# Kernel optimization log

Measured on AMD Instinct MI355X. Metric: run time of the kernel, lower is better.

Reference implementation:

```python
import jax, jax.numpy as jnp
import numpy as np

EPSILON = 0.1
TAU = 1.0
NORM_EPS = 1e-12  # matches torch.nn.functional.normalize eps


def setup_inputs() -> dict:
    key = jax.random.key(0)
    k_ids, k_emb = jax.random.split(key)
    B, T, V, D = 2, 2048, 50257, 768
    input_ids = jax.random.randint(k_ids, (B, T), 0, V, dtype=jnp.int64)
    embedding_weight = jax.random.normal(k_emb, (V, D), dtype=jnp.float32)
    return {"input_ids": input_ids, "embedding_weight": embedding_weight}


def _l2_normalize(x):
    # F.normalize(p=2): x / max(||x||, eps)
    n = jnp.linalg.norm(x, axis=-1, keepdims=True)
    return x / jnp.maximum(n, NORM_EPS)


def reference(input_ids, embedding_weight):
    B, T = input_ids.shape
    V, D = embedding_weight.shape
    # embedding lookup -> (B*T, D)
    vecs = embedding_weight[input_ids].reshape(B * T, D)
    vectors_norm = _l2_normalize(vecs)
    embed_norm = _l2_normalize(embedding_weight)
    # (B*T, V) similarity, scaled by epsilon/2
    scaled_sim = (vectors_norm @ embed_norm.T) * (EPSILON / 2.0)
    # gumbel_softmax (soft, tau=1): softmax((logits + gumbel) / tau)
    gkey = jax.random.key(42)
    gumbel = jax.random.gumbel(gkey, scaled_sim.shape, dtype=scaled_sim.dtype)
    weights = jax.nn.softmax((scaled_sim + gumbel) / TAU, axis=1)
    # mix back through the (unnormalized) embedding table -> (B, T, D)
    selected = weights @ embedding_weight
    return selected.reshape(B, T, D)
```

## Files before the change

### kernel.cpp

```cpp
#include <hip/hip_runtime.h>
#include <stdint.h>

constexpr int VOC  = 50257;
constexpr int VPAD = 50304;
constexpr int DEMB = 768;
constexpr int NQ   = 4096;
constexpr float EPS_HALF = 0.05f;
constexpr float LOG2E = 1.4426950408889634f;
constexpr float C16   = -23.083120654223414f;

typedef __attribute__((ext_vector_type(4))) short    short4_t;
typedef __attribute__((ext_vector_type(8))) short    short8_t;
typedef __attribute__((ext_vector_type(4))) float    float4_t;
typedef __attribute__((ext_vector_type(4))) uint32_t uint4_t;

__device__ __forceinline__ short f2bf(float f) {
  uint32_t u = __float_as_uint(f);
  u += 0x7FFFu + ((u >> 16) & 1u);
  return (short)(u >> 16);
}

__device__ __forceinline__ void tf8(uint32_t e0, uint32_t out[8]) {
  const uint32_t K0 = 0u, K1 = 42u, K2 = 0x1BD11BDAu ^ 42u;
  uint32_t x0[8], x1[8];
#pragma unroll
  for (int r = 0; r < 8; ++r) { x0[r] = K0; x1[r] = e0 + (uint32_t)r + K1; }
#define R8(a) _Pragma("unroll") \
  for (int r = 0; r < 8; ++r) { x0[r] += x1[r]; x1[r] = __builtin_rotateleft32(x1[r], a) ^ x0[r]; }
#define INJ8(a, b, i) _Pragma("unroll") \
  for (int r = 0; r < 8; ++r) { x0[r] += (a); x1[r] += (b) + (uint32_t)(i); }
  R8(13) R8(15) R8(26) R8(6)
  INJ8(K1, K2, 1)
  R8(17) R8(29) R8(16) R8(24)
  INJ8(K2, K0, 2)
  R8(13) R8(15) R8(26) R8(6)
  INJ8(K0, K1, 3)
  R8(17) R8(29) R8(16) R8(24)
  INJ8(K1, K2, 4)
  R8(13) R8(15) R8(26) R8(6)
#pragma unroll
  for (int r = 0; r < 8; ++r) { x0[r] += K2; x1[r] += K0 + 5u; out[r] = x0[r] ^ x1[r]; }
#undef R8
#undef INJ8
}

__device__ __forceinline__ float neg_ln_u(uint32_t bits) {
  uint32_t n = bits >> 9;
  uint32_t m = 8388608u - n;
  float t_log = (23.0f - __builtin_amdgcn_logf((float)n)) * 0.69314718055994531f;
  float x = (float)m * 1.1920928955078125e-7f;
  float t_ser = x * fmaf(x, fmaf(x, fmaf(x, 0.25f, 0.3333333333f), 0.5f), 1.0f);
  return (m < 32768u) ? t_ser : t_log;
}

__global__ void k_prep_e(const float* __restrict__ E, short* __restrict__ Eb,
                         float* __restrict__ rk2) {
  int j = blockIdx.x;
  int t = threadIdx.x;
  __shared__ float red[4];
  float ssq = 0.f;
  if (j < VOC) {
    if (t < 192) {
      float4_t v = *(const float4_t*)(E + (size_t)j * DEMB + t * 4);
      ssq = v[0]*v[0] + v[1]*v[1] + v[2]*v[2] + v[3]*v[3];
      short4_t b; b[0]=f2bf(v[0]); b[1]=f2bf(v[1]); b[2]=f2bf(v[2]); b[3]=f2bf(v[3]);
      *(short4_t*)(Eb + (size_t)j * DEMB + t * 4) = b;
    }
  } else if (t < 192) {
    short4_t z = {0,0,0,0};
    *(short4_t*)(Eb + (size_t)j * DEMB + t * 4) = z;
  }
  for (int off = 32; off; off >>= 1) ssq += __shfl_xor(ssq, off);
  if ((t & 63) == 0) red[t >> 6] = ssq;
  __syncthreads();
  if (t == 0) {
    float s = red[0] + red[1] + red[2] + red[3];
    rk2[j] = (j < VOC) ? (EPS_HALF * LOG2E / fmaxf(sqrtf(s), 1e-12f)) : 0.f;
  }
}

__global__ void k_prep_q(const int* __restrict__ ids, const float* __restrict__ E,
                         short* __restrict__ qn) {
  int p = blockIdx.x;
  int t = threadIdx.x;
  int id = ids[p];
  __shared__ float red[4];
  __shared__ float scale_s;
  float4_t v = {0.f, 0.f, 0.f, 0.f};
  float ssq = 0.f;
  if (t < 192) {
    v = *(const float4_t*)(E + (size_t)id * DEMB + t * 4);
    ssq = v[0]*v[0] + v[1]*v[1] + v[2]*v[2] + v[3]*v[3];
  }
  for (int off = 32; off; off >>= 1) ssq += __shfl_xor(ssq, off);
  if ((t & 63) == 0) red[t >> 6] = ssq;
  __syncthreads();
  if (t == 0) scale_s = 1.0f / fmaxf(sqrtf(red[0]+red[1]+red[2]+red[3]), 1e-12f);
  __syncthreads();
  float sc = scale_s;
  if (t < 192) {
    short4_t b; b[0]=f2bf(v[0]*sc); b[1]=f2bf(v[1]*sc); b[2]=f2bf(v[2]*sc); b[3]=f2bf(v[3]*sc);
    *(short4_t*)(qn + (size_t)p * DEMB + t * 4) = b;
  }
}

__global__ void k_transpose(const short* __restrict__ Eb, short* __restrict__ Et) {
  int lane = threadIdx.x & 63;
  int dg   = threadIdx.x >> 6;
  int key  = blockIdx.x * 64 + lane;
  int d0   = blockIdx.y * 32 + dg * 8;
  short8_t v = *(const short8_t*)(Eb + (size_t)key * DEMB + d0);
#pragma unroll
  for (int q = 0; q < 8; ++q)
    Et[(size_t)(d0 + q) * VPAD + key] = v[q];
}

__global__ void k_zero(float* __restrict__ O, float* __restrict__ lsum) {
  int idx = blockIdx.x * 256 + threadIdx.x;
  if (idx < NQ) lsum[idx] = 0.f;
  float4_t z = {0.f, 0.f, 0.f, 0.f};
  ((float4_t*)O)[idx] = z;
}

__device__ __forceinline__ int swz(int row, int byte) {
  return (row << 7) + (byte ^ ((row & 7) << 4));
}

__device__ __forceinline__ void stage_g2l(short* L, const short* __restrict__ g,
                                          long grow0, long stride, long col0, int tid) {
  int r7 = tid >> 3;
  int c8 = (tid & 7) << 3;
#pragma unroll
  for (int i = 0; i < 4; ++i) {
    int  row = r7 + i * 32;
    long cs  = (long)(c8 ^ ((row & 7) << 3));
    const short* src = g + (grow0 + row) * stride + col0 + cs;
    short* dst = L + row * 64 + c8;
    __builtin_amdgcn_global_load_lds(
        (const __attribute__((address_space(1))) void*)src,
        (__attribute__((address_space(3))) void*)dst, 16, 0, 0);
  }
}

__device__ __forceinline__ short8_t ldfrag(const short* L, int row, int kbyte) {
  return *(const short8_t*)(L + (swz(row, kbyte) >> 1));
}

__global__ __launch_bounds__(256) void k_gemm1(
    const short* __restrict__ qn, const short* __restrict__ Eb,
    _Float16* __restrict__ S, int c0, int KC) {
  __shared__ short lA[128 * 64];
  __shared__ short lB[128 * 64];
  int tid = threadIdx.x, lane = tid & 63;
  int wv = tid >> 6, wr = wv >> 1, wc = wv & 1;
  int rowbase = blockIdx.x * 128;
  int colbase = blockIdx.y * 128;
  float4_t acc[4][4];
  float4_t zero = {0.f, 0.f, 0.f, 0.f};
#pragma unroll
  for (int mt = 0; mt < 4; ++mt)
#pragma unroll
    for (int nt = 0; nt < 4; ++nt) acc[mt][nt] = zero;

  for (int kt = 0; kt < DEMB / 64; ++kt) {
    __syncthreads();
    stage_g2l(lA, qn, rowbase,      DEMB, kt * 64, tid);
    stage_g2l(lB, Eb, c0 + colbase, DEMB, kt * 64, tid);
    __syncthreads();
#pragma unroll
    for (int ks = 0; ks < 2; ++ks) {
      int kb = ks * 64 + (lane >> 4) * 16;
      short8_t a[4], b[4];
#pragma unroll
      for (int mt = 0; mt < 4; ++mt) a[mt] = ldfrag(lA, wr * 64 + mt * 16 + (lane & 15), kb);
#pragma unroll
      for (int nt = 0; nt < 4; ++nt) b[nt] = ldfrag(lB, wc * 64 + nt * 16 + (lane & 15), kb);
#pragma unroll
      for (int mt = 0; mt < 4; ++mt)
#pragma unroll
        for (int nt = 0; nt < 4; ++nt)
          acc[mt][nt] = __builtin_amdgcn_mfma_f32_16x16x32_bf16(a[mt], b[nt], acc[mt][nt], 0, 0, 0);
    }
  }
#pragma unroll
  for (int mt = 0; mt < 4; ++mt) {
    int prow = rowbase + wr * 64 + mt * 16 + ((lane >> 4) << 2);
    int jc0  = colbase + wc * 64 + (lane & 15);
#pragma unroll
    for (int r = 0; r < 4; ++r) {
      _Float16* dst = S + (size_t)(prow + r) * KC + jc0;
#pragma unroll
      for (int nt = 0; nt < 4; ++nt) dst[nt * 16] = (_Float16)acc[mt][nt][r];
    }
  }
}

__global__ __launch_bounds__(256) void k_gumbel(
    uint32_t* __restrict__ SP, const float* __restrict__ rk2,
    float* __restrict__ lsum, int c0, int KCeff, int KC) {
  int p    = blockIdx.x;
  int colq = blockIdx.y * 2048 + threadIdx.x * 8;
  float partial = 0.f;
  if (colq < KCeff) {
    uint32_t* base = SP + ((size_t)p * KC + colq) / 2;
    uint4_t sv = *(const uint4_t*)base;
    int j0 = c0 + colq;
    float4_t rk_lo = *(const float4_t*)(rk2 + j0);
    float4_t rk_hi = *(const float4_t*)(rk2 + j0 + 4);
    uint32_t bits[8];
    tf8((uint32_t)p * (uint32_t)VOC + (uint32_t)j0, bits);
    float pe[8];
#pragma unroll
    for (int i = 0; i < 8; ++i) {
      uint32_t h = (sv[i >> 1] >> ((i & 1) * 16)) & 0xFFFFu;
      _Float16 hf = *(_Float16*)&h;
      float simf = (float)hf;
      float rkj = (i < 4) ? rk_lo[i] : rk_hi[i - 4];
      float t = neg_ln_u(bits[i]);
      float v = __builtin_amdgcn_exp2f(fmaf(simf, rkj, C16)) * __builtin_amdgcn_rcpf(t);
      bool ok = (j0 + i) < VOC;
      pe[i] = ok ? v : 0.f;
      partial += pe[i];
    }
    uint4_t pkv;
#pragma unroll
    for (int i = 0; i < 4; ++i) {
      uint32_t r;
      asm("v_cvt_pk_bf16_f32 %0, %1, %2" : "=v"(r) : "v"(pe[2 * i]), "v"(pe[2 * i + 1]));
      pkv[i] = r;
    }
    *(uint4_t*)base = pkv;
  }
  for (int off = 32; off; off >>= 1) partial += __shfl_xor(partial, off);
  if ((threadIdx.x & 63) == 0 && partial != 0.f) unsafeAtomicAdd(&lsum[p], partial);
}

__global__ __launch_bounds__(256) void k_gemm2(
    const short* __restrict__ P, const short* __restrict__ Et,
    float* __restrict__ O, int c0, int KC, int kseg) {
  __shared__ short lA[2][128 * 64];
  __shared__ short lB[2][128 * 64];
  int tid = threadIdx.x, lane = tid & 63;
  int wv = tid >> 6, wr = wv >> 1, wc = wv & 1;
  int rowbase = blockIdx.x * 128;
  int colbase = blockIdx.y * 128;
  int kbase   = blockIdx.z * kseg;
  float4_t acc[4][4];
  float4_t zero = {0.f, 0.f, 0.f, 0.f};
#pragma unroll
  for (int mt = 0; mt < 4; ++mt)
#pragma unroll
    for (int nt = 0; nt < 4; ++nt) acc[mt][nt] = zero;

  int nt_steps = kseg / 64;
  stage_g2l(lA[0], P,  rowbase, KC,   kbase, tid);
  stage_g2l(lB[0], Et, colbase, VPAD, (long)c0 + kbase, tid);

  for (int kt = 0; kt < nt_steps; ++kt) {
    __syncthreads();
    int cur = kt & 1;
    if (kt + 1 < nt_steps) {
      stage_g2l(lA[cur ^ 1], P,  rowbase, KC,   kbase + (kt + 1) * 64, tid);
      stage_g2l(lB[cur ^ 1], Et, colbase, VPAD, (long)c0 + kbase + (kt + 1) * 64, tid);
    }
#pragma unroll
    for (int ks = 0; ks < 2; ++ks) {
      int kb = ks * 64 + (lane >> 4) * 16;
      short8_t a[4], b[4];
#pragma unroll
      for (int mt = 0; mt < 4; ++mt) a[mt] = ldfrag(lA[cur], wr * 64 + mt * 16 + (lane & 15), kb);
#pragma unroll
      for (int nt = 0; nt < 4; ++nt) b[nt] = ldfrag(lB[cur], wc * 64 + nt * 16 + (lane & 15), kb);
#pragma unroll
      for (int mt = 0; mt < 4; ++mt)
#pragma unroll
        for (int nt = 0; nt < 4; ++nt)
          acc[mt][nt] = __builtin_amdgcn_mfma_f32_16x16x32_bf16(a[mt], b[nt], acc[mt][nt], 0, 0, 0);
    }
  }
#pragma unroll
  for (int mt = 0; mt < 4; ++mt)
#pragma unroll
    for (int nt = 0; nt < 4; ++nt) {
      int d = colbase + wc * 64 + nt * 16 + (lane & 15);
#pragma unroll
      for (int r = 0; r < 4; ++r) {
        int p = rowbase + wr * 64 + mt * 16 + ((lane >> 4) << 2) + r;
        unsafeAtomicAdd(&O[(size_t)p * DEMB + d], acc[mt][nt][r]);
      }
    }
}

__global__ void k_finalize(const float* __restrict__ O, const float* __restrict__ lsum,
                           float* __restrict__ out) {
  int idx = blockIdx.x * 256 + threadIdx.x;
  float inv = 1.0f / lsum[idx / 192];
  float4_t v = ((const float4_t*)O)[idx];
  v[0]*=inv; v[1]*=inv; v[2]*=inv; v[3]*=inv;
  ((float4_t*)out)[idx] = v;
}

extern "C" void kernel_launch(void* const* d_in, const int* in_sizes, int n_in,
                              void* d_out, int out_size, void* d_ws, size_t ws_size,
                              hipStream_t stream) {
  (void)in_sizes; (void)n_in; (void)out_size;
  const int*   ids = (const int*)d_in[0];
  const float* E   = (const float*)d_in[1];
  float*       out = (float*)d_out;

  char* w = (char*)d_ws;
  short* Eb = (short*)w;      w += (size_t)VPAD * DEMB * 2;
  short* Et = (short*)w;      w += (size_t)DEMB * VPAD * 2;
  short* qn = (short*)w;      w += (size_t)NQ * DEMB * 2;
  float* O  = (float*)w;      w += (size_t)NQ * DEMB * 4;
  float* rk2 = (float*)w;     w += (size_t)VPAD * 4;
  float* lsum = (float*)w;    w += NQ * 4;
  void*  SP = (void*)w;
  size_t fixed = (size_t)(w - (char*)d_ws);

  int KC = 2048;
  if      (fixed + (size_t)NQ * 8192 * 2 <= ws_size) KC = 8192;
  else if (fixed + (size_t)NQ * 4096 * 2 <= ws_size) KC = 4096;
  int chunks = (VPAD + KC - 1) / KC;

  k_zero<<<(NQ * DEMB / 4) / 256, 256, 0, stream>>>(O, lsum);
  k_prep_e<<<VPAD, 256, 0, stream>>>(E, Eb, rk2);
  k_prep_q<<<NQ, 256, 0, stream>>>(ids, E, qn);
  k_transpose<<<dim3(VPAD / 64, DEMB / 32), 256, 0, stream>>>(Eb, Et);

  for (int c = 0; c < chunks; ++c) {
    int c0 = c * KC;
    int KCeff = VPAD - c0; if (KCeff > KC) KCeff = KC;
    k_gemm1<<<dim3(NQ / 128, KCeff / 128), 256, 0, stream>>>(qn, Eb, (_Float16*)SP, c0, KC);
    k_gumbel<<<dim3(NQ, (KCeff + 2047) / 2048), 256, 0, stream>>>(
        (uint32_t*)SP, rk2, lsum, c0, KCeff, KC);
    int KS = 4;
    while (KS > 1 && (KCeff % (KS * 64)) != 0) KS >>= 1;
    k_gemm2<<<dim3(NQ / 128, DEMB / 128, KS), 256, 0, stream>>>(
        (const short*)SP, Et, O, c0, KC, KCeff / KS);
  }
  k_finalize<<<(NQ * DEMB / 4) / 256, 256, 0, stream>>>(O, lsum, out);
}
```

Measured before the change: 1.562 ms.

## Enlarge GEMM tiles to 256 rows with 512-thread blocks and double-buffered LDS

Both GEMMs move to 512-thread blocks with 256-row tiles held in dynamic LDS. gemm1 gains double-buffered async global-to-LDS staging with explicit vmcnt waits in place of two full syncthreads per step. gemm2 uses an 8-way K split. VPAD is padded to 50688 so chunks divide evenly into 256-column tiles. The intent is more reuse per LDS load and better overlap of loads with MFMA, at the cost of more LDS per block (up to 128 KB), lower occupancy, extra barriers, and more padded work and atomics.

New measurement: 1.726 ms. 1.1x slower.

```diff
diff --git a/kernel.cpp b/kernel.cpp
--- a/kernel.cpp
+++ b/kernel.cpp
@@ -2,7 +2,7 @@
 #include <stdint.h>
 
 constexpr int VOC  = 50257;
-constexpr int VPAD = 50304;
+constexpr int VPAD = 50688;
 constexpr int DEMB = 768;
 constexpr int NQ   = 4096;
 constexpr float EPS_HALF = 0.05f;
@@ -13,6 +13,8 @@
 typedef __attribute__((ext_vector_type(8))) short    short8_t;
 typedef __attribute__((ext_vector_type(4))) float    float4_t;
 typedef __attribute__((ext_vector_type(4))) uint32_t uint4_t;
+
+#define VMW(N) asm volatile("s_waitcnt vmcnt(" #N ")" ::: "memory")
 
 __device__ __forceinline__ short f2bf(float f) {
   uint32_t u = __float_as_uint(f);
@@ -126,13 +128,14 @@
   return (row << 7) + (byte ^ ((row & 7) << 4));
 }
 
-__device__ __forceinline__ void stage_g2l(short* L, const short* __restrict__ g,
-                                          long grow0, long stride, long col0, int tid) {
-  int r7 = tid >> 3;
+template<int PASSES>
+__device__ __forceinline__ void stage512(short* L, const short* __restrict__ g,
+                                         long grow0, long stride, long col0, int tid) {
   int c8 = (tid & 7) << 3;
-#pragma unroll
-  for (int i = 0; i < 4; ++i) {
-    int  row = r7 + i * 32;
+  int r0 = tid >> 3;
+#pragma unroll
+  for (int i = 0; i < PASSES; ++i) {
+    int  row = r0 + i * 64;
     long cs  = (long)(c8 ^ ((row & 7) << 3));
     const short* src = g + (grow0 + row) * stride + col0 + cs;
     short* dst = L + row * 64 + c8;
@@ -146,46 +149,69 @@
   return *(const short8_t*)(L + (swz(row, kbyte) >> 1));
 }
 
-__global__ __launch_bounds__(256) void k_gemm1(
+__device__ __forceinline__ float4_t mfma16(short8_t a, short8_t b, float4_t c) {
+  return __builtin_amdgcn_mfma_f32_16x16x32_bf16(a, b, c, 0, 0, 0);
+}
+
+__global__ __launch_bounds__(512) void k_gemm1(
     const short* __restrict__ qn, const short* __restrict__ Eb,
     _Float16* __restrict__ S, int c0, int KC) {
-  __shared__ short lA[128 * 64];
-  __shared__ short lB[128 * 64];
+  extern __shared__ short lds[];
+  short* A0 = lds;
+  short* B0 = lds + 2 * 256 * 64;
   int tid = threadIdx.x, lane = tid & 63;
-  int wv = tid >> 6, wr = wv >> 1, wc = wv & 1;
-  int rowbase = blockIdx.x * 128;
-  int colbase = blockIdx.y * 128;
-  float4_t acc[4][4];
+  int wid = tid >> 6, wm = wid >> 2, wn = wid & 3;
+  int rowbase = blockIdx.x * 256;
+  long colg   = (long)c0 + blockIdx.y * 256;
+  float4_t acc[8][4];
   float4_t zero = {0.f, 0.f, 0.f, 0.f};
 #pragma unroll
-  for (int mt = 0; mt < 4; ++mt)
+  for (int mt = 0; mt < 8; ++mt)
 #pragma unroll
     for (int nt = 0; nt < 4; ++nt) acc[mt][nt] = zero;
 
-  for (int kt = 0; kt < DEMB / 64; ++kt) {
-    __syncthreads();
-    stage_g2l(lA, qn, rowbase,      DEMB, kt * 64, tid);
-    stage_g2l(lB, Eb, c0 + colbase, DEMB, kt * 64, tid);
-    __syncthreads();
+  const int n = DEMB / 64;
+  stage512<4>(A0, qn, rowbase, DEMB, 0, tid);
+  stage512<4>(B0, Eb, colg,    DEMB, 0, tid);
+  for (int kt = 0; kt < n; ++kt) {
+    int cur = kt & 1;
+    if (kt + 1 < n) {
+      stage512<4>(A0 + (cur ^ 1) * (256 * 64), qn, rowbase, DEMB, (kt + 1) * 64, tid);
+      stage512<4>(B0 + (cur ^ 1) * (256 * 64), Eb, colg,    DEMB, (kt + 1) * 64, tid);
+      VMW(8);
+    } else {
+      VMW(0);
+    }
+    __builtin_amdgcn_s_barrier();
+    const short* Al = A0 + cur * (256 * 64);
+    const short* Bl = B0 + cur * (256 * 64);
 #pragma unroll
     for (int ks = 0; ks < 2; ++ks) {
       int kb = ks * 64 + (lane >> 4) * 16;
-      short8_t a[4], b[4];
-#pragma unroll
-      for (int mt = 0; mt < 4; ++mt) a[mt] = ldfrag(lA, wr * 64 + mt * 16 + (lane & 15), kb);
-#pragma unroll
-      for (int nt = 0; nt < 4; ++nt) b[nt] = ldfrag(lB, wc * 64 + nt * 16 + (lane & 15), kb);
-#pragma unroll
-      for (int mt = 0; mt < 4; ++mt)
-#pragma unroll
-        for (int nt = 0; nt < 4; ++nt)
-          acc[mt][nt] = __builtin_amdgcn_mfma_f32_16x16x32_bf16(a[mt], b[nt], acc[mt][nt], 0, 0, 0);
-    }
-  }
-#pragma unroll
-  for (int mt = 0; mt < 4; ++mt) {
-    int prow = rowbase + wr * 64 + mt * 16 + ((lane >> 4) << 2);
-    int jc0  = colbase + wc * 64 + (lane & 15);
+      short8_t b4[4];
+#pragma unroll
+      for (int nt = 0; nt < 4; ++nt) b4[nt] = ldfrag(Bl, wn * 64 + nt * 16 + (lane & 15), kb);
+#pragma unroll
+      for (int mh = 0; mh < 2; ++mh) {
+        short8_t a4[4];
+#pragma unroll
+        for (int j = 0; j < 4; ++j)
+          a4[j] = ldfrag(Al, wm * 128 + mh * 64 + j * 16 + (lane & 15), kb);
+        __builtin_amdgcn_s_setprio(1);
+#pragma unroll
+        for (int j = 0; j < 4; ++j)
+#pragma unroll
+          for (int nt = 0; nt < 4; ++nt)
+            acc[mh * 4 + j][nt] = mfma16(a4[j], b4[nt], acc[mh * 4 + j][nt]);
+        __builtin_amdgcn_s_setprio(0);
+        __builtin_amdgcn_s_barrier();
+      }
+    }
+  }
+#pragma unroll
+  for (int mt = 0; mt < 8; ++mt) {
+    int prow = rowbase + wm * 128 + mt * 16 + ((lane >> 4) << 2);
+    int jc0  = blockIdx.y * 256 + wn * 64 + (lane & 15);
 #pragma unroll
     for (int r = 0; r < 4; ++r) {
       _Float16* dst = S + (size_t)(prow + r) * KC + jc0;
@@ -235,57 +261,70 @@
   if ((threadIdx.x & 63) == 0 && partial != 0.f) unsafeAtomicAdd(&lsum[p], partial);
 }
 
-__global__ __launch_bounds__(256) void k_gemm2(
+__global__ __launch_bounds__(512) void k_gemm2(
     const short* __restrict__ P, const short* __restrict__ Et,
     float* __restrict__ O, int c0, int KC, int kseg) {
-  __shared__ short lA[2][128 * 64];
-  __shared__ short lB[2][128 * 64];
+  extern __shared__ short lds[];
+  short* A0 = lds;
+  short* B0 = lds + 2 * 256 * 64;
   int tid = threadIdx.x, lane = tid & 63;
-  int wv = tid >> 6, wr = wv >> 1, wc = wv & 1;
-  int rowbase = blockIdx.x * 128;
+  int wid = tid >> 6, wm = wid >> 2, wn = wid & 3;
+  int rowbase = blockIdx.x * 256;
   int colbase = blockIdx.y * 128;
-  int kbase   = blockIdx.z * kseg;
-  float4_t acc[4][4];
+  long kbase  = (long)blockIdx.z * kseg;
+  float4_t acc[8][2];
   float4_t zero = {0.f, 0.f, 0.f, 0.f};
 #pragma unroll
-  for (int mt = 0; mt < 4; ++mt)
-#pragma unroll
-    for (int nt = 0; nt < 4; ++nt) acc[mt][nt] = zero;
-
-  int nt_steps = kseg / 64;
-  stage_g2l(lA[0], P,  rowbase, KC,   kbase, tid);
-  stage_g2l(lB[0], Et, colbase, VPAD, (long)c0 + kbase, tid);
-
-  for (int kt = 0; kt < nt_steps; ++kt) {
-    __syncthreads();
+  for (int mt = 0; mt < 8; ++mt)
+#pragma unroll
+    for (int nt = 0; nt < 2; ++nt) acc[mt][nt] = zero;
+
+  const int n = kseg / 64;
+  stage512<4>(A0, P,  rowbase, KC,   kbase, tid);
+  stage512<2>(B0, Et, colbase, VPAD, (long)c0 + kbase, tid);
+  for (int kt = 0; kt < n; ++kt) {
     int cur = kt & 1;
-    if (kt + 1 < nt_steps) {
-      stage_g2l(lA[cur ^ 1], P,  rowbase, KC,   kbase + (kt + 1) * 64, tid);
-      stage_g2l(lB[cur ^ 1], Et, colbase, VPAD, (long)c0 + kbase + (kt + 1) * 64, tid);
-    }
+    if (kt + 1 < n) {
+      stage512<4>(A0 + (cur ^ 1) * (256 * 64), P,  rowbase, KC,   kbase + (kt + 1) * 64, tid);
+      stage512<2>(B0 + (cur ^ 1) * (128 * 64), Et, colbase, VPAD, (long)c0 + kbase + (kt + 1) * 64, tid);
+      VMW(6);
+    } else {
+      VMW(0);
+    }
+    __builtin_amdgcn_s_barrier();
+    const short* Al = A0 + cur * (256 * 64);
+    const short* Bl = B0 + cur * (128 * 64);
 #pragma unroll
     for (int ks = 0; ks < 2; ++ks) {
       int kb = ks * 64 + (lane >> 4) * 16;
-      short8_t a[4], b[4];
-#pragma unroll
-      for (int mt = 0; mt < 4; ++mt) a[mt] = ldfrag(lA[cur], wr * 64 + mt * 16 + (lane & 15), kb);
-#pragma unroll
-      for (int nt = 0; nt < 4; ++nt) b[nt] = ldfrag(lB[cur], wc * 64 + nt * 16 + (lane & 15), kb);
-#pragma unroll
-      for (int mt = 0; mt < 4; ++mt)
-#pragma unroll
-        for (int nt = 0; nt < 4; ++nt)
-          acc[mt][nt] = __builtin_amdgcn_mfma_f32_16x16x32_bf16(a[mt], b[nt], acc[mt][nt], 0, 0, 0);
-    }
-  }
-#pragma unroll
-  for (int mt = 0; mt < 4; ++mt)
-#pragma unroll
-    for (int nt = 0; nt < 4; ++nt) {
-      int d = colbase + wc * 64 + nt * 16 + (lane & 15);
+      short8_t b2[2];
+#pragma unroll
+      for (int nt = 0; nt < 2; ++nt) b2[nt] = ldfrag(Bl, wn * 32 + nt * 16 + (lane & 15), kb);
+#pragma unroll
+      for (int mh = 0; mh < 2; ++mh) {
+        short8_t a4[4];
+#pragma unroll
+        for (int j = 0; j < 4; ++j)
+          a4[j] = ldfrag(Al, wm * 128 + mh * 64 + j * 16 + (lane & 15), kb);
+        __builtin_amdgcn_s_setprio(1);
+#pragma unroll
+        for (int j = 0; j < 4; ++j)
+#pragma unroll
+          for (int nt = 0; nt < 2; ++nt)
+            acc[mh * 4 + j][nt] = mfma16(a4[j], b2[nt], acc[mh * 4 + j][nt]);
+        __builtin_amdgcn_s_setprio(0);
+        __builtin_amdgcn_s_barrier();
+      }
+    }
+  }
+#pragma unroll
+  for (int mt = 0; mt < 8; ++mt)
+#pragma unroll
+    for (int nt = 0; nt < 2; ++nt) {
+      int d = colbase + wn * 32 + nt * 16 + (lane & 15);
 #pragma unroll
       for (int r = 0; r < 4; ++r) {
-        int p = rowbase + wr * 64 + mt * 16 + ((lane >> 4) << 2) + r;
+        int p = rowbase + wm * 128 + mt * 16 + ((lane >> 4) << 2) + r;
         unsafeAtomicAdd(&O[(size_t)p * DEMB + d], acc[mt][nt][r]);
       }
     }
@@ -307,6 +346,9 @@
   const int*   ids = (const int*)d_in[0];
   const float* E   = (const float*)d_in[1];
   float*       out = (float*)d_out;
+
+  hipFuncSetAttribute((const void*)k_gemm1, hipFuncAttributeMaxDynamicSharedMemorySize, 128 * 1024);
+  hipFuncSetAttribute((const void*)k_gemm2, hipFuncAttributeMaxDynamicSharedMemorySize, 96 * 1024);
 
   char* w = (char*)d_ws;
   short* Eb = (short*)w;      w += (size_t)VPAD * DEMB * 2;
@@ -331,13 +373,13 @@
   for (int c = 0; c < chunks; ++c) {
     int c0 = c * KC;
     int KCeff = VPAD - c0; if (KCeff > KC) KCeff = KC;
-    k_gemm1<<<dim3(NQ / 128, KCeff / 128), 256, 0, stream>>>(qn, Eb, (_Float16*)SP, c0, KC);
+    k_gemm1<<<dim3(NQ / 256, KCeff / 256), 512, 128 * 1024, stream>>>(
+        qn, Eb, (_Float16*)SP, c0, KC);
     k_gumbel<<<dim3(NQ, (KCeff + 2047) / 2048), 256, 0, stream>>>(
         (uint32_t*)SP, rk2, lsum, c0, KCeff, KC);
-    int KS = 4;
-    while (KS > 1 && (KCeff % (KS * 64)) != 0) KS >>= 1;
-    k_gemm2<<<dim3(NQ / 128, DEMB / 128, KS), 256, 0, stream>>>(
-        (const short*)SP, Et, O, c0, KC, KCeff / KS);
+    int kseg = KCeff / 8;
+    k_gemm2<<<dim3(NQ / 256, DEMB / 128, 8), 512, 96 * 1024, stream>>>(
+        (const short*)SP, Et, O, c0, KC, kseg);
   }
   k_finalize<<<(NQ * DEMB / 4) / 256, 256, 0, stream>>>(O, lsum, out);
 }
```
